# Kernel tuning notes

Hardware: AMD Instinct MI355X
Metric: run time of the kernel (lower is better)

The kernel has to match this reference:

```python
import jax, jax.numpy as jnp
import numpy as np

EPS = 1e-5

def _bn(x, g, b, axes):
    m = jnp.mean(x, axes, keepdims=True)
    v = jnp.var(x, axes, keepdims=True)
    return (x - m) * jax.lax.rsqrt(v + EPS) * g + b

def _fps(p, m):
    # farthest point sampling: p [B,N,3] -> int32 indices [B,m]
    B, N, _ = p.shape
    def step(carry, _):
        mind, last = carry
        lastp = jnp.take_along_axis(p, last[:, None, None], axis=1)[:, 0]  # [B,3]
        d = jnp.sum((p - lastp[:, None, :]) ** 2, axis=-1)                 # [B,N]
        mind = jnp.minimum(mind, d)
        nxt = jnp.argmax(mind, axis=1).astype(jnp.int32)
        return (mind, nxt), last
    init = (jnp.full((B, N), jnp.inf, p.dtype), jnp.zeros((B,), jnp.int32))
    _, idxs = jax.lax.scan(step, init, None, length=m)  # [m,B]
    return idxs.T

def _gather(x, idx):
    # x [B,N,C], idx [B,...] -> [B,...,C]
    B, C = x.shape[0], x.shape[-1]
    flat = idx.reshape(B, -1)
    out = jnp.take_along_axis(x, flat[:, :, None], axis=1)
    return out.reshape(idx.shape + (C,))

def _transition_down(p, h, W, g, b, stride, nsample):
    # p [B,N,3], h [B,N,C] -> new_p [B,N//stride,3], y [B,N//stride,Cout]
    B, N, _ = p.shape
    M = N // stride
    idx = _fps(p, M)
    new_p = _gather(p, idx)                                               # [B,M,3]
    d = jnp.sum((new_p[:, :, None, :] - p[:, None, :, :]) ** 2, axis=-1)  # [B,M,N]
    _, nidx = jax.lax.top_k(-d, nsample)                                  # [B,M,k]
    gp = _gather(p, nidx) - new_p[:, :, None, :]                          # rel xyz [B,M,k,3]
    gx = _gather(h, nidx)                                                 # [B,M,k,C]
    feat = jnp.concatenate([gp, gx], axis=-1)                             # with_xyz=True
    y = jnp.einsum('bmkc,cd->bmkd', feat, W)
    y = jax.nn.relu(_bn(y, g, b, (0, 1, 2)))
    return new_p, jnp.max(y, axis=2)                                      # MaxPool1d(nsample)

def _forward(x, W1, g1, b1, W2, g2, b2, W3, g3, b3, W4, g4, b4, W5, g5, b5,
             Wc1, bc1, gc1, hc1, Wc2, bc2, gc2, hc2, Wc3, bc3):
    p = x[..., :3]                                    # in_channels == 3 -> features = xyz
    h = jnp.einsum('bnc,cd->bnd', p, W1)
    h = jax.nn.relu(_bn(h, g1, b1, (0, 1)))           # enc1: stride=1
    p, h = _transition_down(p, h, W2, g2, b2, 4, 16)  # enc2
    p, h = _transition_down(p, h, W3, g3, b3, 4, 16)  # enc3
    p, h = _transition_down(p, h, W4, g4, b4, 4, 16)  # enc4
    p, h = _transition_down(p, h, W5, g5, b5, 4, 16)  # enc5
    z = jnp.mean(h, axis=1)                           # segment-mean pool -> [B,512]
    z = jax.nn.relu(_bn(z @ Wc1 + bc1, gc1, hc1, (0,)))   # Dropout = identity (eval)
    z = jax.nn.relu(_bn(z @ Wc2 + bc2, gc2, hc2, (0,)))
    return z @ Wc3 + bc3                              # [B,40]

def setup_inputs() -> dict:
    key = jax.random.key(0)
    ks = jax.random.split(key, 16)
    B, N = 16, 4096
    def lin(k, fi, fo):
        return (jax.random.normal(k, (fi, fo), jnp.float32) / np.sqrt(fi)).astype(jnp.float32)
    inp = {"x": jax.random.normal(ks[0], (B, N, 3), jnp.float32)}
    planes = [32, 64, 128, 256, 512]
    ins = [3, 3 + 32, 3 + 64, 3 + 128, 3 + 256]
    for i, (fi, fo) in enumerate(zip(ins, planes), start=1):
        inp[f"W{i}"] = lin(ks[i], fi, fo)
        inp[f"g{i}"] = jnp.ones((fo,), jnp.float32)
        inp[f"b{i}"] = jnp.zeros((fo,), jnp.float32)
    dims = [(512, 256), (256, 128), (128, 40)]
    for j, (fi, fo) in enumerate(dims, start=1):
        inp[f"Wc{j}"] = lin(ks[5 + j], fi, fo)
        inp[f"bc{j}"] = jnp.zeros((fo,), jnp.float32)
        if j < 3:
            inp[f"gc{j}"] = jnp.ones((fo,), jnp.float32)
            inp[f"hc{j}"] = jnp.zeros((fo,), jnp.float32)
    return inp

def reference(x, W1, g1, b1, W2, g2, b2, W3, g3, b3, W4, g4, b4, W5, g5, b5,
              Wc1, bc1, gc1, hc1, Wc2, bc2, gc2, hc2, Wc3, bc3):
    return _forward(x, W1, g1, b1, W2, g2, b2, W3, g3, b3, W4, g4, b4, W5, g5, b5,
                    Wc1, bc1, gc1, hc1, Wc2, bc2, gc2, hc2, Wc3, bc3)
```

## Files before the change

kernel.cpp:

```cpp
#include <hip/hip_runtime.h>
#include <math.h>
#include <float.h>

#define BN_EPS 1e-5f

__device__ __forceinline__ float sqdist_exact(float dx, float dy, float dz) {
  return __fadd_rn(__fadd_rn(__fmul_rn(dx, dx), __fmul_rn(dy, dy)), __fmul_rn(dz, dz));
}

__global__ void __launch_bounds__(256) mlp1_kernel(const float* __restrict__ x,
                                                   const float* __restrict__ W1,
                                                   float* __restrict__ h1, int rows) {
  int tid = blockIdx.x * 256 + threadIdx.x;
  int row = tid >> 5;
  int d = tid & 31;
  if (row >= rows) return;
  float x0 = x[row * 3 + 0], x1 = x[row * 3 + 1], x2 = x[row * 3 + 2];
  float acc = x0 * W1[d] + x1 * W1[32 + d] + x2 * W1[64 + d];
  h1[row * 32 + d] = acc;
}

__global__ void stats_kernel(const float* __restrict__ v, int n, int D,
                             float* __restrict__ partial) {
  int tid = blockIdx.x * blockDim.x + threadIdx.x;
  int stride = blockDim.x * gridDim.x;
  float s = 0.f, q = 0.f;
  for (int i = tid; i < n; i += stride) { float a = v[i]; s += a; q += a * a; }
  int c = tid % D;
  extern __shared__ float sm[];
  for (int i = threadIdx.x; i < 2 * D; i += blockDim.x) sm[i] = 0.f;
  __syncthreads();
  atomicAdd(&sm[c], s);
  atomicAdd(&sm[D + c], q);
  __syncthreads();
  for (int i = threadIdx.x; i < 2 * D; i += blockDim.x)
    atomicAdd(&partial[(blockIdx.x & 63) * 2 * D + i], sm[i]);
}

__global__ void finalize_kernel(const float* __restrict__ partial,
                                const float* __restrict__ g, const float* __restrict__ b,
                                float cnt, int D, float* __restrict__ ss) {
  int d = threadIdx.x;
  if (d >= D) return;
  float s = 0.f, q = 0.f;
  for (int j = 0; j < 64; j++) { s += partial[j * 2 * D + d]; q += partial[j * 2 * D + D + d]; }
  float mean = s / cnt;
  float var = q / cnt - mean * mean;
  var = fmaxf(var, 0.f);
  float sc = g[d] * rsqrtf(var + BN_EPS);
  ss[d] = sc;
  ss[D + d] = b[d] - mean * sc;
}

__global__ void bn_apply_kernel(float* __restrict__ vmax, const float* __restrict__ vmin,
                                const float* __restrict__ ss, int D, int n) {
  int tid = blockIdx.x * blockDim.x + threadIdx.x;
  int stride = blockDim.x * gridDim.x;
  for (int i = tid; i < n; i += stride) {
    int d = i % D;
    float sc = ss[d], sh = ss[D + d];
    float v = (sc >= 0.f) ? vmax[i] : vmin[i];
    vmax[i] = fmaxf(v * sc + sh, 0.f);
  }
}

#define DPP_STEP(CTRL)                                                                   \
  {                                                                                      \
    unsigned int nhi = (unsigned int)__builtin_amdgcn_update_dpp((int)khi, (int)khi,     \
                                                                 CTRL, 0xf, 0xf, false); \
    unsigned int nlo = (unsigned int)__builtin_amdgcn_update_dpp((int)klo, (int)klo,     \
                                                                 CTRL, 0xf, 0xf, false); \
    unsigned long long nk = (((unsigned long long)nhi) << 32) | nlo;                     \
    if (nk > wk) { wk = nk; khi = nhi; klo = nlo; }                                      \
  }

template <int P, int NW>
__device__ __forceinline__ void fps_body(const float* __restrict__ pb,
                                         float* __restrict__ newp_b,
                                         float* spts, float* snew,
                                         unsigned long long* slots, int t) {
  constexpr int BS = NW * 64;
  constexpr int N = P * BS;
  constexpr int M = N / 4;
  const int wv = t >> 6;
  const int lane = t & 63;
  float px[P], py[P], pz[P], md[P];
#pragma unroll
  for (int j = 0; j < P; j++) {
    int i = j * BS + t;
    float x = pb[3 * i], y = pb[3 * i + 1], z = pb[3 * i + 2];
    px[j] = x; py[j] = y; pz[j] = z; md[j] = INFINITY;
    spts[3 * i] = x; spts[3 * i + 1] = y; spts[3 * i + 2] = z;
  }
  float lx = pb[0], ly = pb[1], lz = pb[2];
  if (t == 0) {
    if constexpr (NW > 1) {
      snew[0] = lx; snew[1] = ly; snew[2] = lz;
    } else {
      newp_b[0] = lx; newp_b[1] = ly; newp_b[2] = lz;
    }
  }

  for (int r = 1; r < M; r++) {
    float bv; int bi;
    {
      float d0 = sqdist_exact(px[0] - lx, py[0] - ly, pz[0] - lz);
      float m0 = fminf(md[0], d0);
      md[0] = m0;
      bv = m0; bi = t;
    }
#pragma unroll
    for (int j = 1; j < P; j++) {
      float d = sqdist_exact(px[j] - lx, py[j] - ly, pz[j] - lz);
      float m = fminf(md[j], d);
      md[j] = m;
      if (m > bv) { bv = m; bi = j * BS + t; }
    }
    unsigned int khi = __float_as_uint(bv);
    unsigned int klo = ~(unsigned int)bi;
    unsigned long long wk = (((unsigned long long)khi) << 32) | klo;
    DPP_STEP(0x111);
    DPP_STEP(0x112);
    DPP_STEP(0x114);
    DPP_STEP(0x118);
    DPP_STEP(0x142);
    DPP_STEP(0x143);
    unsigned int gidx;
    if constexpr (NW == 1) {
      unsigned int wlo = (unsigned int)__builtin_amdgcn_readlane((int)wk, 63);
      gidx = ~wlo;
    } else {
      unsigned long long* base = slots + (r & 1) * NW;
      if (lane == 63) base[wv] = wk;
      __syncthreads();
      unsigned long long fk = base[0];
#pragma unroll
      for (int w = 1; w < NW; w++) {
        unsigned long long k2 = base[w];
        if (k2 > fk) fk = k2;
      }
      gidx = ~(unsigned int)fk;
    }
    lx = spts[3 * gidx];
    ly = spts[3 * gidx + 1];
    lz = spts[3 * gidx + 2];
    if (t == 0) {
      if constexpr (NW > 1) {
        snew[3 * r] = lx; snew[3 * r + 1] = ly; snew[3 * r + 2] = lz;
      } else {
        newp_b[3 * r] = lx; newp_b[3 * r + 1] = ly; newp_b[3 * r + 2] = lz;
      }
    }
  }
  if constexpr (NW > 1) {
    __syncthreads();
    for (int i = t; i < M * 3; i += BS) newp_b[i] = snew[i];
  }
}

template <int P, int NW>
__global__ void __launch_bounds__(NW * 64) fps4_kernel(const float* __restrict__ p,
                                                       float* __restrict__ newp) {
  constexpr int BS = NW * 64;
  constexpr int N = P * BS;
  constexpr int M = N / 4;
  __shared__ float spts[N * 3];
  __shared__ float snew[NW > 1 ? M * 3 : 1];
  __shared__ unsigned long long slots[NW > 1 ? 2 * NW : 2];
  fps_body<P, NW>(p + (size_t)blockIdx.x * N * 3, newp + (size_t)blockIdx.x * M * 3,
                  spts, snew, slots, threadIdx.x);
}

__device__ __forceinline__ void knn_body(const float* __restrict__ p,
                                         const float* __restrict__ newp,
                                         int N, int M, int BM,
                                         int* __restrict__ nidx,
                                         int gwid, int lane) {
  if (gwid >= BM) return;
  int b = gwid / M;
  const float* pb = p + (size_t)b * N * 3;
  float qx = newp[(size_t)gwid * 3], qy = newp[(size_t)gwid * 3 + 1], qz = newp[(size_t)gwid * 3 + 2];
  float bd[16];
  int bi[16];
#pragma unroll
  for (int s = 0; s < 16; s++) { bd[s] = INFINITY; bi[s] = 0x7FFFFFFF; }
  for (int c = lane; c < N; c += 64) {
    float d = sqdist_exact(pb[3 * c] - qx, pb[3 * c + 1] - qy, pb[3 * c + 2] - qz);
    if (d < bd[15]) {
      bd[15] = d; bi[15] = c;
#pragma unroll
      for (int s = 15; s >= 1; --s) {
        bool sw = bd[s] < bd[s - 1];
        if (sw) {
          float tf = bd[s]; bd[s] = bd[s - 1]; bd[s - 1] = tf;
          int ti = bi[s]; bi[s] = bi[s - 1]; bi[s - 1] = ti;
        }
      }
    }
  }
  int out = 0;
  for (int r = 0; r < 16; r++) {
    float v = bd[0]; int ii = bi[0];
    float mv = v; int mi = ii;
#pragma unroll
    for (int m = 1; m < 64; m <<= 1) {
      float v2 = __shfl_xor(mv, m);
      int i2 = __shfl_xor(mi, m);
      if (v2 < mv || (v2 == mv && i2 < mi)) { mv = v2; mi = i2; }
    }
    if (mi == ii) {
#pragma unroll
      for (int s = 0; s < 15; s++) { bd[s] = bd[s + 1]; bi[s] = bi[s + 1]; }
      bd[15] = INFINITY; bi[15] = 0x7FFFFFFF;
    }
    if (lane == r) out = mi;
  }
  if (lane < 16) nidx[(size_t)gwid * 16 + lane] = out;
}

__global__ void __launch_bounds__(256) knn_kernel(const float* __restrict__ p,
                                                  const float* __restrict__ newp,
                                                  int N, int M, int BM,
                                                  int* __restrict__ nidx) {
  int gwid = (blockIdx.x * 256 + threadIdx.x) >> 6;
  int lane = threadIdx.x & 63;
  knn_body(p, newp, N, M, BM, nidx, gwid, lane);
}

template <int P, int NW>
__global__ void __launch_bounds__(256) fused_fps_knn_kernel(
    const float* __restrict__ fp, float* __restrict__ fnewp,
    const float* __restrict__ kp, const float* __restrict__ knewp,
    int kN, int kM, int kBM, int* __restrict__ knidx) {
  constexpr int BS = NW * 64;
  constexpr int N = P * BS;
  constexpr int M = N / 4;
  __shared__ float spts[N * 3];
  __shared__ float snew[NW > 1 ? M * 3 : 1];
  __shared__ unsigned long long slots[NW > 1 ? 2 * NW : 2];
  const int t = threadIdx.x;
  if (blockIdx.x < 16) {
    if (NW > 1 || t < 64) {
      fps_body<P, NW>(fp + (size_t)blockIdx.x * N * 3, fnewp + (size_t)blockIdx.x * M * 3,
                      spts, snew, slots, t);
    }
  } else {
    int gwid = ((blockIdx.x - 16) * 256 + t) >> 6;
    int lane = t & 63;
    knn_body(kp, knewp, kN, kM, kBM, knidx, gwid, lane);
  }
}

__global__ void __launch_bounds__(256) gemm_kernel(
    const float* __restrict__ p, const float* __restrict__ h, const float* __restrict__ newp,
    const int* __restrict__ nidx, const float* __restrict__ W,
    float* __restrict__ ymax, float* __restrict__ ymin, float* __restrict__ partial,
    int N, int M, int BM, int Ch, int Cpad, int D, int Gseq) {
  extern __shared__ float sm[];
  int Ctot = Ch + 3;
  int TD = D < 256 ? D : 256;
  int Gpar = 256 / TD;
  float* sfeat = sm;
  float* sstat = sm + Gpar * 16 * Cpad;
  int t = threadIdx.x;
  for (int i = t; i < 2 * D; i += 256) sstat[i] = 0.f;
  int mloc = t / TD;
  int dbase = t % TD;
  int DV = D / TD;
  __syncthreads();
  for (int s = 0; s < Gseq; s++) {
    int grp0 = (blockIdx.x * Gseq + s) * Gpar;
    if (grp0 >= BM) break;
    int nf = Gpar * 16 * Cpad;
    for (int i = t; i < nf; i += 256) {
      int c = i % Cpad;
      int rk = i / Cpad;
      int k = rk & 15;
      int g = rk >> 4;
      int grp = grp0 + g;
      float val = 0.f;
      if (grp < BM && c < Ctot) {
        int b = grp / M;
        int nb = nidx[(size_t)grp * 16 + k];
        if (c < 3)
          val = p[((size_t)b * N + nb) * 3 + c] - newp[(size_t)grp * 3 + c];
        else
          val = h[((size_t)b * N + nb) * Ch + (c - 3)];
      }
      sfeat[i] = val;
    }
    __syncthreads();
    int grp = grp0 + mloc;
    bool act = grp < BM;
    const float* fr = sfeat + mloc * 16 * Cpad;
    for (int dv = 0; dv < DV; ++dv) {
      int d = dbase + (dv << 8);
      float acc[16];
#pragma unroll
      for (int k = 0; k < 16; k++) acc[k] = 0.f;
      for (int c = 0; c < Cpad; c += 4) {
        float w0 = (c < Ctot) ? W[(size_t)c * D + d] : 0.f;
        float w1 = (c + 1 < Ctot) ? W[(size_t)(c + 1) * D + d] : 0.f;
        float w2 = (c + 2 < Ctot) ? W[(size_t)(c + 2) * D + d] : 0.f;
        float w3 = (c + 3 < Ctot) ? W[(size_t)(c + 3) * D + d] : 0.f;
#pragma unroll
        for (int k = 0; k < 16; k++) {
          const float4 f = *reinterpret_cast<const float4*>(fr + k * Cpad + c);
          acc[k] += f.x * w0 + f.y * w1 + f.z * w2 + f.w * w3;
        }
      }
      if (act) {
        float ssum = 0.f, ssq = 0.f, amax = -INFINITY, amin = INFINITY;
#pragma unroll
        for (int k = 0; k < 16; k++) {
          float a = acc[k];
          ssum += a; ssq += a * a;
          amax = fmaxf(amax, a); amin = fminf(amin, a);
        }
        ymax[(size_t)grp * D + d] = amax;
        ymin[(size_t)grp * D + d] = amin;
        atomicAdd(&sstat[d], ssum);
        atomicAdd(&sstat[D + d], ssq);
      }
    }
    __syncthreads();
  }
  for (int i = t; i < 2 * D; i += 256)
    atomicAdd(&partial[(blockIdx.x & 63) * 2 * D + i], sstat[i]);
}

__global__ void __launch_bounds__(512) classifier_kernel(
    const float* __restrict__ h4,
    const float* __restrict__ Wc1, const float* __restrict__ bc1,
    const float* __restrict__ gc1, const float* __restrict__ hc1,
    const float* __restrict__ Wc2, const float* __restrict__ bc2,
    const float* __restrict__ gc2, const float* __restrict__ hc2,
    const float* __restrict__ Wc3, const float* __restrict__ bc3,
    float* __restrict__ out) {
  __shared__ float z[16 * 512];
  __shared__ float z1[16 * 256];
  __shared__ float z2[16 * 128];
  __shared__ float sc[256], sh[256];
  int t = threadIdx.x;
  for (int i = t; i < 16 * 512; i += 512) {
    int b = i >> 9, c = i & 511;
    float s = 0.f;
    for (int k = 0; k < 16; k++) s += h4[((size_t)b * 16 + k) * 512 + c];
    z[i] = s * (1.f / 16.f);
  }
  __syncthreads();
  for (int i = t; i < 16 * 256; i += 512) {
    int b = i >> 8, d = i & 255;
    float a = bc1[d];
    for (int c = 0; c < 512; c++) a += z[(b << 9) + c] * Wc1[c * 256 + d];
    z1[i] = a;
  }
  __syncthreads();
  if (t < 256) {
    float s = 0.f, q = 0.f;
    for (int b = 0; b < 16; b++) { float a = z1[(b << 8) + t]; s += a; q += a * a; }
    float mean = s * (1.f / 16.f);
    float var = fmaxf(q * (1.f / 16.f) - mean * mean, 0.f);
    float scl = gc1[t] * rsqrtf(var + BN_EPS);
    sc[t] = scl; sh[t] = hc1[t] - mean * scl;
  }
  __syncthreads();
  for (int i = t; i < 16 * 256; i += 512) {
    int d = i & 255;
    z1[i] = fmaxf(z1[i] * sc[d] + sh[d], 0.f);
  }
  __syncthreads();
  for (int i = t; i < 16 * 128; i += 512) {
    int b = i >> 7, d = i & 127;
    float a = bc2[d];
    for (int c = 0; c < 256; c++) a += z1[(b << 8) + c] * Wc2[c * 128 + d];
    z2[i] = a;
  }
  __syncthreads();
  if (t < 128) {
    float s = 0.f, q = 0.f;
    for (int b = 0; b < 16; b++) { float a = z2[(b << 7) + t]; s += a; q += a * a; }
    float mean = s * (1.f / 16.f);
    float var = fmaxf(q * (1.f / 16.f) - mean * mean, 0.f);
    float scl = gc2[t] * rsqrtf(var + BN_EPS);
    sc[t] = scl; sh[t] = hc2[t] - mean * scl;
  }
  __syncthreads();
  for (int i = t; i < 16 * 128; i += 512) {
    int d = i & 127;
    z2[i] = fmaxf(z2[i] * sc[d] + sh[d], 0.f);
  }
  __syncthreads();
  for (int i = t; i < 640; i += 512) {
    int b = i / 40, d = i % 40;
    float a = bc3[d];
    for (int c = 0; c < 128; c++) a += z2[(b << 7) + c] * Wc3[c * 40 + d];
    out[i] = a;
  }
}

extern "C" void kernel_launch(void* const* d_in, const int* in_sizes, int n_in,
                              void* d_out, int out_size, void* d_ws, size_t ws_size,
                              hipStream_t stream) {
  (void)in_sizes; (void)n_in; (void)out_size; (void)ws_size;
  const float* x   = (const float*)d_in[0];
  const float* W1  = (const float*)d_in[1];
  const float* g1  = (const float*)d_in[2];
  const float* b1  = (const float*)d_in[3];
  const float* W2  = (const float*)d_in[4];
  const float* g2  = (const float*)d_in[5];
  const float* b2  = (const float*)d_in[6];
  const float* W3  = (const float*)d_in[7];
  const float* g3  = (const float*)d_in[8];
  const float* b3  = (const float*)d_in[9];
  const float* W4  = (const float*)d_in[10];
  const float* g4  = (const float*)d_in[11];
  const float* b4  = (const float*)d_in[12];
  const float* W5  = (const float*)d_in[13];
  const float* g5  = (const float*)d_in[14];
  const float* b5  = (const float*)d_in[15];
  const float* Wc1 = (const float*)d_in[16];
  const float* bc1 = (const float*)d_in[17];
  const float* gc1 = (const float*)d_in[18];
  const float* hc1 = (const float*)d_in[19];
  const float* Wc2 = (const float*)d_in[20];
  const float* bc2 = (const float*)d_in[21];
  const float* gc2 = (const float*)d_in[22];
  const float* hc2 = (const float*)d_in[23];
  const float* Wc3 = (const float*)d_in[24];
  const float* bc3 = (const float*)d_in[25];
  float* out = (float*)d_out;

  float* ws = (float*)d_ws;
  float* HA   = ws;
  float* HB   = HA + 2097152;
  float* YMIN = HB + 1048576;
  float* NP1  = YMIN + 1048576;
  float* NP2  = NP1 + 49152;
  float* NP3  = NP2 + 12288;
  float* NP4  = NP3 + 3072;
  int*   NIDX = (int*)(NP4 + 768);
  float* PART = (float*)(NIDX + 262144);
  float* SS   = PART + 5 * 65536;

  hipMemsetAsync(PART, 0, 5 * 65536 * sizeof(float), stream);

  mlp1_kernel<<<(65536 * 32) / 256, 256, 0, stream>>>(x, W1, HA, 65536);
  stats_kernel<<<256, 256, 2 * 32 * sizeof(float), stream>>>(HA, 65536 * 32, 32, PART);
  finalize_kernel<<<1, 32, 0, stream>>>(PART, g1, b1, 65536.f, 32, SS);
  bn_apply_kernel<<<512, 256, 0, stream>>>(HA, HA, SS, 32, 65536 * 32);

  fps4_kernel<16, 4><<<16, 256, 0, stream>>>(x, NP1);
  fused_fps_knn_kernel<4, 4><<<16 + 4096, 256, 0, stream>>>(
      NP1, NP2, x, NP1, 4096, 1024, 16384, NIDX);
  gemm_kernel<<<512, 256, (4 * 16 * 36 + 2 * 64) * sizeof(float), stream>>>(
      x, HA, NP1, NIDX, W2, HB, YMIN, PART + 65536, 4096, 1024, 16384, 32, 36, 64, 8);
  finalize_kernel<<<1, 64, 0, stream>>>(PART + 65536, g2, b2, (float)(16384 * 16), 64, SS + 1024);
  bn_apply_kernel<<<512, 256, 0, stream>>>(HB, YMIN, SS + 1024, 64, 16384 * 64);

  fused_fps_knn_kernel<4, 1><<<16 + 1024, 256, 0, stream>>>(
      NP2, NP3, NP1, NP2, 1024, 256, 4096, NIDX);
  gemm_kernel<<<512, 256, (2 * 16 * 68 + 2 * 128) * sizeof(float), stream>>>(
      NP1, HB, NP2, NIDX, W3, HA, YMIN, PART + 2 * 65536, 1024, 256, 4096, 64, 68, 128, 4);
  finalize_kernel<<<1, 128, 0, stream>>>(PART + 2 * 65536, g3, b3, (float)(4096 * 16), 128, SS + 2048);
  bn_apply_kernel<<<512, 256, 0, stream>>>(HA, YMIN, SS + 2048, 128, 4096 * 128);

  fused_fps_knn_kernel<1, 1><<<16 + 256, 256, 0, stream>>>(
      NP3, NP4, NP2, NP3, 256, 64, 1024, NIDX);
  gemm_kernel<<<512, 256, (16 * 132 + 2 * 256) * sizeof(float), stream>>>(
      NP2, HA, NP3, NIDX, W4, HB, YMIN, PART + 3 * 65536, 256, 64, 1024, 128, 132, 256, 2);
  finalize_kernel<<<1, 256, 0, stream>>>(PART + 3 * 65536, g4, b4, (float)(1024 * 16), 256, SS + 3072);
  bn_apply_kernel<<<512, 256, 0, stream>>>(HB, YMIN, SS + 3072, 256, 1024 * 256);

  knn_kernel<<<(256 + 3) / 4, 256, 0, stream>>>(NP3, NP4, 64, 16, 256, NIDX);
  gemm_kernel<<<256, 256, (16 * 260 + 2 * 512) * sizeof(float), stream>>>(
      NP3, HB, NP4, NIDX, W5, HA, YMIN, PART + 4 * 65536, 64, 16, 256, 256, 260, 512, 1);
  finalize_kernel<<<1, 512, 0, stream>>>(PART + 4 * 65536, g5, b5, (float)(256 * 16), 512, SS + 4096);
  bn_apply_kernel<<<512, 256, 0, stream>>>(HA, YMIN, SS + 4096, 512, 256 * 512);

  classifier_kernel<<<1, 512, 0, stream>>>(HA, Wc1, bc1, gc1, hc1, Wc2, bc2, gc2, hc2, Wc3, bc3, out);
}
```

Measured before the change: 1.439 ms.

## Fuse next-stage FPS and kNN blocks into current-stage gather-GEMM launch

The per-stage gather-GEMM is merged with the next stage's farthest-point sampling and kNN into one heterogeneous launch. Block ranges choose which body runs, and separate neighbour-index buffers per stage let the next kNN write while the current GEMM reads. This overlaps the serial FPS blocks with parallel GEMM work and removes separate launches. In exchange, every block in the fused kernel reserves the FPS static shared memory on top of the GEMM shared memory, which may lower occupancy.

```diff
diff --git a/kernel.cpp b/kernel.cpp
--- a/kernel.cpp
+++ b/kernel.cpp
@@ -218,58 +218,24 @@
   if (lane < 16) nidx[(size_t)gwid * 16 + lane] = out;
 }
 
-__global__ void __launch_bounds__(256) knn_kernel(const float* __restrict__ p,
-                                                  const float* __restrict__ newp,
-                                                  int N, int M, int BM,
-                                                  int* __restrict__ nidx) {
-  int gwid = (blockIdx.x * 256 + threadIdx.x) >> 6;
-  int lane = threadIdx.x & 63;
-  knn_body(p, newp, N, M, BM, nidx, gwid, lane);
-}
-
-template <int P, int NW>
-__global__ void __launch_bounds__(256) fused_fps_knn_kernel(
-    const float* __restrict__ fp, float* __restrict__ fnewp,
-    const float* __restrict__ kp, const float* __restrict__ knewp,
-    int kN, int kM, int kBM, int* __restrict__ knidx) {
-  constexpr int BS = NW * 64;
-  constexpr int N = P * BS;
-  constexpr int M = N / 4;
-  __shared__ float spts[N * 3];
-  __shared__ float snew[NW > 1 ? M * 3 : 1];
-  __shared__ unsigned long long slots[NW > 1 ? 2 * NW : 2];
-  const int t = threadIdx.x;
-  if (blockIdx.x < 16) {
-    if (NW > 1 || t < 64) {
-      fps_body<P, NW>(fp + (size_t)blockIdx.x * N * 3, fnewp + (size_t)blockIdx.x * M * 3,
-                      spts, snew, slots, t);
-    }
-  } else {
-    int gwid = ((blockIdx.x - 16) * 256 + t) >> 6;
-    int lane = t & 63;
-    knn_body(kp, knewp, kN, kM, kBM, knidx, gwid, lane);
-  }
-}
-
-__global__ void __launch_bounds__(256) gemm_kernel(
-    const float* __restrict__ p, const float* __restrict__ h, const float* __restrict__ newp,
-    const int* __restrict__ nidx, const float* __restrict__ W,
-    float* __restrict__ ymax, float* __restrict__ ymin, float* __restrict__ partial,
-    int N, int M, int BM, int Ch, int Cpad, int D, int Gseq) {
-  extern __shared__ float sm[];
+__device__ __forceinline__ void gemm_body(
+    float* sm, const float* __restrict__ p, const float* __restrict__ h,
+    const float* __restrict__ newp, const int* __restrict__ nidx,
+    const float* __restrict__ W, float* __restrict__ ymax, float* __restrict__ ymin,
+    float* __restrict__ partial, int N, int M, int BM, int Ch, int Cpad, int D,
+    int Gseq, int bid, int t) {
   int Ctot = Ch + 3;
   int TD = D < 256 ? D : 256;
   int Gpar = 256 / TD;
   float* sfeat = sm;
   float* sstat = sm + Gpar * 16 * Cpad;
-  int t = threadIdx.x;
   for (int i = t; i < 2 * D; i += 256) sstat[i] = 0.f;
   int mloc = t / TD;
   int dbase = t % TD;
   int DV = D / TD;
   __syncthreads();
   for (int s = 0; s < Gseq; s++) {
-    int grp0 = (blockIdx.x * Gseq + s) * Gpar;
+    int grp0 = (bid * Gseq + s) * Gpar;
     if (grp0 >= BM) break;
     int nf = Gpar * 16 * Cpad;
     for (int i = t; i < nf; i += 256) {
@@ -326,7 +292,75 @@
     __syncthreads();
   }
   for (int i = t; i < 2 * D; i += 256)
-    atomicAdd(&partial[(blockIdx.x & 63) * 2 * D + i], sstat[i]);
+    atomicAdd(&partial[(bid & 63) * 2 * D + i], sstat[i]);
+}
+
+template <int P, int NW>
+__global__ void __launch_bounds__(256) fused_fps_knn_kernel(
+    const float* __restrict__ fp, float* __restrict__ fnewp,
+    const float* __restrict__ kp, const float* __restrict__ knewp,
+    int kN, int kM, int kBM, int* __restrict__ knidx) {
+  constexpr int BS = NW * 64;
+  constexpr int N = P * BS;
+  constexpr int M = N / 4;
+  __shared__ float spts[N * 3];
+  __shared__ float snew[NW > 1 ? M * 3 : 1];
+  __shared__ unsigned long long slots[NW > 1 ? 2 * NW : 2];
+  const int t = threadIdx.x;
+  if (blockIdx.x < 16) {
+    if (NW > 1 || t < 64) {
+      fps_body<P, NW>(fp + (size_t)blockIdx.x * N * 3, fnewp + (size_t)blockIdx.x * M * 3,
+                      spts, snew, slots, t);
+    }
+  } else {
+    int gwid = ((blockIdx.x - 16) * 256 + t) >> 6;
+    int lane = t & 63;
+    knn_body(kp, knewp, kN, kM, kBM, knidx, gwid, lane);
+  }
+}
+
+template <int P, int NW>
+__global__ void __launch_bounds__(256) fused_gfk_kernel(
+    const float* __restrict__ p, const float* __restrict__ h,
+    const float* __restrict__ newp, const int* __restrict__ nidx,
+    const float* __restrict__ W, float* __restrict__ ymax, float* __restrict__ ymin,
+    float* __restrict__ partial, int N, int M, int BM, int Ch, int Cpad, int D,
+    int Gseq, int nGemm,
+    const float* __restrict__ fp, float* __restrict__ fnewp, int nFps,
+    const float* __restrict__ kp, const float* __restrict__ knewp,
+    int kN, int kM, int kBM, int* __restrict__ knidx) {
+  constexpr int FBS = NW * 64;
+  constexpr int FN = P * FBS;
+  constexpr int FM = FN / 4;
+  __shared__ float spts[FN * 3];
+  __shared__ float snew[NW > 1 ? FM * 3 : 1];
+  __shared__ unsigned long long slots[NW > 1 ? 2 * NW : 2];
+  extern __shared__ float sm[];
+  const int t = threadIdx.x;
+  const int bid = blockIdx.x;
+  if (bid < nGemm) {
+    gemm_body(sm, p, h, newp, nidx, W, ymax, ymin, partial,
+              N, M, BM, Ch, Cpad, D, Gseq, bid, t);
+  } else if (bid < nGemm + nFps) {
+    int fb = bid - nGemm;
+    if (NW > 1 || t < 64) {
+      fps_body<P, NW>(fp + (size_t)fb * FN * 3, fnewp + (size_t)fb * FM * 3,
+                      spts, snew, slots, t);
+    }
+  } else {
+    int gwid = ((bid - nGemm - nFps) * 256 + t) >> 6;
+    knn_body(kp, knewp, kN, kM, kBM, knidx, gwid, t & 63);
+  }
+}
+
+__global__ void __launch_bounds__(256) gemm_kernel(
+    const float* __restrict__ p, const float* __restrict__ h, const float* __restrict__ newp,
+    const int* __restrict__ nidx, const float* __restrict__ W,
+    float* __restrict__ ymax, float* __restrict__ ymin, float* __restrict__ partial,
+    int N, int M, int BM, int Ch, int Cpad, int D, int Gseq) {
+  extern __shared__ float sm[];
+  gemm_body(sm, p, h, newp, nidx, W, ymax, ymin, partial,
+            N, M, BM, Ch, Cpad, D, Gseq, blockIdx.x, threadIdx.x);
 }
 
 __global__ void __launch_bounds__(512) classifier_kernel(
@@ -432,16 +466,19 @@
   float* out = (float*)d_out;
 
   float* ws = (float*)d_ws;
-  float* HA   = ws;
-  float* HB   = HA + 2097152;
-  float* YMIN = HB + 1048576;
-  float* NP1  = YMIN + 1048576;
-  float* NP2  = NP1 + 49152;
-  float* NP3  = NP2 + 12288;
-  float* NP4  = NP3 + 3072;
-  int*   NIDX = (int*)(NP4 + 768);
-  float* PART = (float*)(NIDX + 262144);
-  float* SS   = PART + 5 * 65536;
+  float* HA    = ws;
+  float* HB    = HA + 2097152;
+  float* YMIN  = HB + 1048576;
+  float* NP1   = YMIN + 1048576;
+  float* NP2   = NP1 + 49152;
+  float* NP3   = NP2 + 12288;
+  float* NP4   = NP3 + 3072;
+  int*   NIDX1 = (int*)(NP4 + 768);
+  int*   NIDX2 = NIDX1 + 262144;
+  int*   NIDX3 = NIDX2 + 65536;
+  int*   NIDX4 = NIDX3 + 16384;
+  float* PART  = (float*)(NIDX4 + 4096);
+  float* SS    = PART + 5 * 65536;
 
   hipMemsetAsync(PART, 0, 5 * 65536 * sizeof(float), stream);
 
@@ -452,29 +489,31 @@
 
   fps4_kernel<16, 4><<<16, 256, 0, stream>>>(x, NP1);
   fused_fps_knn_kernel<4, 4><<<16 + 4096, 256, 0, stream>>>(
-      NP1, NP2, x, NP1, 4096, 1024, 16384, NIDX);
-  gemm_kernel<<<512, 256, (4 * 16 * 36 + 2 * 64) * sizeof(float), stream>>>(
-      x, HA, NP1, NIDX, W2, HB, YMIN, PART + 65536, 4096, 1024, 16384, 32, 36, 64, 8);
+      NP1, NP2, x, NP1, 4096, 1024, 16384, NIDX1);
+
+  fused_gfk_kernel<4, 1><<<512 + 16 + 1024, 256, (4 * 16 * 36 + 2 * 64) * sizeof(float), stream>>>(
+      x, HA, NP1, NIDX1, W2, HB, YMIN, PART + 65536, 4096, 1024, 16384, 32, 36, 64, 8, 512,
+      NP2, NP3, 16,
+      NP1, NP2, 1024, 256, 4096, NIDX2);
   finalize_kernel<<<1, 64, 0, stream>>>(PART + 65536, g2, b2, (float)(16384 * 16), 64, SS + 1024);
   bn_apply_kernel<<<512, 256, 0, stream>>>(HB, YMIN, SS + 1024, 64, 16384 * 64);
 
-  fused_fps_knn_kernel<4, 1><<<16 + 1024, 256, 0, stream>>>(
-      NP2, NP3, NP1, NP2, 1024, 256, 4096, NIDX);
-  gemm_kernel<<<512, 256, (2 * 16 * 68 + 2 * 128) * sizeof(float), stream>>>(
-      NP1, HB, NP2, NIDX, W3, HA, YMIN, PART + 2 * 65536, 1024, 256, 4096, 64, 68, 128, 4);
+  fused_gfk_kernel<1, 1><<<512 + 16 + 256, 256, (2 * 16 * 68 + 2 * 128) * sizeof(float), stream>>>(
+      NP1, HB, NP2, NIDX2, W3, HA, YMIN, PART + 2 * 65536, 1024, 256, 4096, 64, 68, 128, 4, 512,
+      NP3, NP4, 16,
+      NP2, NP3, 256, 64, 1024, NIDX3);
   finalize_kernel<<<1, 128, 0, stream>>>(PART + 2 * 65536, g3, b3, (float)(4096 * 16), 128, SS + 2048);
   bn_apply_kernel<<<512, 256, 0, stream>>>(HA, YMIN, SS + 2048, 128, 4096 * 128);
 
-  fused_fps_knn_kernel<1, 1><<<16 + 256, 256, 0, stream>>>(
-      NP3, NP4, NP2, NP3, 256, 64, 1024, NIDX);
-  gemm_kernel<<<512, 256, (16 * 132 + 2 * 256) * sizeof(float), stream>>>(
-      NP2, HA, NP3, NIDX, W4, HB, YMIN, PART + 3 * 65536, 256, 64, 1024, 128, 132, 256, 2);
+  fused_gfk_kernel<1, 1><<<512 + 0 + 64, 256, (16 * 132 + 2 * 256) * sizeof(float), stream>>>(
+      NP2, HA, NP3, NIDX3, W4, HB, YMIN, PART + 3 * 65536, 256, 64, 1024, 128, 132, 256, 2, 512,
+      nullptr, nullptr, 0,
+      NP3, NP4, 64, 16, 256, NIDX4);
   finalize_kernel<<<1, 256, 0, stream>>>(PART + 3 * 65536, g4, b4, (float)(1024 * 16), 256, SS + 3072);
   bn_apply_kernel<<<512, 256, 0, stream>>>(HB, YMIN, SS + 3072, 256, 1024 * 256);
 
-  knn_kernel<<<(256 + 3) / 4, 256, 0, stream>>>(NP3, NP4, 64, 16, 256, NIDX);
   gemm_kernel<<<256, 256, (16 * 260 + 2 * 512) * sizeof(float), stream>>>(
-      NP3, HB, NP4, NIDX, W5, HA, YMIN, PART + 4 * 65536, 64, 16, 256, 256, 260, 512, 1);
+      NP3, HB, NP4, NIDX4, W5, HA, YMIN, PART + 4 * 65536, 64, 16, 256, 256, 260, 512, 1);
   finalize_kernel<<<1, 512, 0, stream>>>(PART + 4 * 65536, g5, b5, (float)(256 * 16), 512, SS + 4096);
   bn_apply_kernel<<<512, 256, 0, stream>>>(HA, YMIN, SS + 4096, 512, 256 * 512);
 
```

Result: faster. 1.378 ms (-4.2%).
